# Optimization experiments

Measured on AMD Instinct MI355X. Metric: run time of the kernel, lower is better.

The kernel has to match this reference:

```python
import jax, jax.numpy as jnp
import numpy as np


def _prelu(x, alpha):
    # PReLU with alpha shared over H,W (per-channel alpha, shape (C,))
    return jnp.where(x >= 0, x, alpha * x)


def _maxpool_2x2_s1_same(x):
    # TF MaxPooling2D(pool_size=2, strides=1, padding='same'): pad bottom/right
    return jax.lax.reduce_window(
        x, -jnp.inf, jax.lax.max,
        window_dimensions=(1, 2, 2, 1), window_strides=(1, 1, 1, 1),
        padding=[(0, 0), (0, 1), (0, 1), (0, 0)])


def _down_sample(x, W, b, alpha):
    # 1x1 Conv2D stride 2 'same' == subsample then channel matmul
    y = jnp.einsum('bhwc,cd->bhwd', x[:, ::2, ::2, :], W) + b
    y = _prelu(y, alpha)
    return _maxpool_2x2_s1_same(y)


def _up_sample(x, W, b, alpha):
    # 1x1 Conv2DTranspose stride 2 'same': even positions get conv output, rest only bias
    B, H, Wd, C = x.shape
    y = jnp.einsum('bhwc,cd->bhwd', x, W)
    z = jnp.zeros((B, 2 * H, 2 * Wd, C), dtype=x.dtype).at[:, ::2, ::2, :].set(y) + b
    z = _prelu(z, alpha)
    return _maxpool_2x2_s1_same(z)


def setup_inputs() -> dict:
    key = jax.random.key(0)
    ks = jax.random.split(key, 12)
    B, H, C = 8, 512, 3
    return {
        'input1': jax.random.normal(ks[0], (B, 2 * H, 2 * H, C), jnp.float32),
        'input2': jax.random.normal(ks[1], (B, H, H, C), jnp.float32),
        'input3': jax.random.normal(ks[2], (B, H // 2, H // 2, C), jnp.float32),
        'W_down': jax.random.normal(ks[3], (C, C), jnp.float32) * 0.5,
        'b_down': jax.random.normal(ks[4], (C,), jnp.float32) * 0.1,
        'alpha_down': jax.random.uniform(ks[5], (C,), jnp.float32) * 0.25,
        'W_up': jax.random.normal(ks[6], (C, C), jnp.float32) * 0.5,
        'b_up': jax.random.normal(ks[7], (C,), jnp.float32) * 0.1,
        'alpha_up': jax.random.uniform(ks[8], (C,), jnp.float32) * 0.25,
        'W_c': jax.random.normal(ks[9], (C, C), jnp.float32) * 0.5,
        'b_c': jax.random.normal(ks[10], (C,), jnp.float32) * 0.1,
        'alpha_g': jax.random.uniform(ks[11], (C,), jnp.float32) * 0.25,
        'scale': 2,
    }


def reference(input1, input2, input3, W_down, b_down, alpha_down,
              W_up, b_up, alpha_up, W_c, b_c, alpha_g, scale):
    assert scale == 2, 'only scale=2 path is well-defined in the source'
    i1 = _down_sample(input1, W_down, b_down, alpha_down)  # (B,H,W,C)
    i2 = input2
    i3 = _up_sample(input3, W_up, b_up, alpha_up)          # (B,H,W,C)

    s = i1 + i2 + i3
    g = jnp.mean(s, axis=(1, 2), keepdims=True)            # GlobalAvgPool, (B,1,1,C)

    conv1x1 = lambda t: jnp.einsum('bhwc,cd->bhwd', t, W_c) + b_c
    x = _prelu(conv1x1(g), alpha_g)
    # self.conv2d is the SAME layer applied three times -> c1 == c2 == c3,
    # hence y1 == y2 == y3; compute once (identical math).
    y = jax.nn.softmax(conv1x1(x), axis=-1)                # (B,1,1,C)
    return y * i1 + y * i2 + y * i3
```

## Files before the change

kernel.cpp:

```cpp
#include <hip/hip_runtime.h>

#define HW 512
#define PITCH 200

__device__ __forceinline__ float prelu(float x, float a) { return x >= 0.f ? x : a * x; }

template<int MODE>
__global__ __launch_bounds__(256, 4) void pass_kernel(
    const float* __restrict__ in1, const float* __restrict__ in2, const float* __restrict__ in3,
    const float* __restrict__ Wd, const float* __restrict__ bd, const float* __restrict__ ad,
    const float* __restrict__ Wu, const float* __restrict__ bu, const float* __restrict__ au,
    float* __restrict__ partials,
    const float* __restrict__ Wc, const float* __restrict__ bc, const float* __restrict__ ag,
    float* __restrict__ out)
{
    __shared__ float d1[17 * PITCH];
    __shared__ float red[4][3];
    __shared__ float ybuf[3];

    const int tid   = threadIdx.x;
    const int bx    = blockIdx.x;
    const int by    = blockIdx.y;
    const int batch = blockIdx.z;
    const int h0    = by * 16;
    const int w0b   = bx * 64;

    if (MODE == 1 && tid < 64) {
        const float* pw = partials + batch * 256 * 3;
        float g0 = 0.f, g1 = 0.f, g2 = 0.f;
        #pragma unroll
        for (int k = 0; k < 4; ++k) {
            const float* p = pw + (tid + 64 * k) * 3;
            g0 += p[0]; g1 += p[1]; g2 += p[2];
        }
        #pragma unroll
        for (int off = 32; off > 0; off >>= 1) {
            g0 += __shfl_down(g0, off);
            g1 += __shfl_down(g1, off);
            g2 += __shfl_down(g2, off);
        }
        if (tid == 0) {
            const float inv_n = 1.f / (float)(HW * HW);
            g0 *= inv_n; g1 *= inv_n; g2 *= inv_n;
            const float x0 = prelu(g0 * Wc[0] + g1 * Wc[3] + g2 * Wc[6] + bc[0], ag[0]);
            const float x1 = prelu(g0 * Wc[1] + g1 * Wc[4] + g2 * Wc[7] + bc[1], ag[1]);
            const float x2 = prelu(g0 * Wc[2] + g1 * Wc[5] + g2 * Wc[8] + bc[2], ag[2]);
            const float q0 = x0 * Wc[0] + x1 * Wc[3] + x2 * Wc[6] + bc[0];
            const float q1 = x0 * Wc[1] + x1 * Wc[4] + x2 * Wc[7] + bc[1];
            const float q2 = x0 * Wc[2] + x1 * Wc[5] + x2 * Wc[8] + bc[2];
            const float m  = fmaxf(q0, fmaxf(q1, q2));
            const float e0 = expf(q0 - m), e1 = expf(q1 - m), e2 = expf(q2 - m);
            const float inv = 1.f / (e0 + e1 + e2);
            ybuf[0] = e0 * inv; ybuf[1] = e1 * inv; ybuf[2] = e2 * inv;
        }
    }

    float wd[9], wu[9];
    #pragma unroll
    for (int k = 0; k < 9; k++) { wd[k] = Wd[k]; wu[k] = Wu[k]; }
    const float bd0 = bd[0], bd1 = bd[1], bd2 = bd[2];
    const float ad0 = ad[0], ad1 = ad[1], ad2 = ad[2];
    const float bu0 = bu[0], bu1 = bu[1], bu2 = bu[2];
    const float au0 = au[0], au1 = au[1], au2 = au[2];
    const float cu0 = prelu(bu0, au0), cu1 = prelu(bu1, au1), cu2 = prelu(bu2, au2);

    #pragma unroll
    for (int step = 0; step < 2; ++step) {
        const int r = step ? 16 : (tid >> 4);
        const int g = step ? tid : (tid & 15);
        if (step == 0 || tid < 16) {
            const int gh  = h0 + r;
            const int ghc = gh < HW ? gh : (HW - 1);
            const float* rb = in1 + ((size_t)(batch * 1024 + 2 * ghc)) * 3072;
            const int px0 = 2 * w0b + 8 * g;
            const float4* lp = reinterpret_cast<const float4*>(rb + (size_t)px0 * 3);
            float arr[28];
            #pragma unroll
            for (int k = 0; k < 7; ++k)
                *reinterpret_cast<float4*>(&arr[4 * k]) = lp[k];

            const bool rowOOR = (gh >= HW);
            float* q = d1 + r * PITCH + 12 * g;
            #pragma unroll
            for (int j = 0; j < 4; ++j) {
                const float x0 = arr[6 * j], x1 = arr[6 * j + 1], x2 = arr[6 * j + 2];
                float v0 = prelu(x0 * wd[0] + x1 * wd[3] + x2 * wd[6] + bd0, ad0);
                float v1 = prelu(x0 * wd[1] + x1 * wd[4] + x2 * wd[7] + bd1, ad1);
                float v2 = prelu(x0 * wd[2] + x1 * wd[5] + x2 * wd[8] + bd2, ad2);
                q[3 * j + 0] = rowOOR ? -INFINITY : v0;
                q[3 * j + 1] = rowOOR ? -INFINITY : v1;
                q[3 * j + 2] = rowOOR ? -INFINITY : v2;
            }
            if (g == 15) {
                const float x0 = arr[24], x1 = arr[25], x2 = arr[26];
                float v0 = prelu(x0 * wd[0] + x1 * wd[3] + x2 * wd[6] + bd0, ad0);
                float v1 = prelu(x0 * wd[1] + x1 * wd[4] + x2 * wd[7] + bd1, ad1);
                float v2 = prelu(x0 * wd[2] + x1 * wd[5] + x2 * wd[8] + bd2, ad2);
                const bool oor = rowOOR || (w0b + 64 >= HW);
                q[12] = oor ? -INFINITY : v0;
                q[13] = oor ? -INFINITY : v1;
                q[14] = oor ? -INFINITY : v2;
            }
        }
    }
    __syncthreads();

    const int r  = tid >> 4;
    const int cg = tid & 15;
    const int h  = h0 + r;
    const int w0 = w0b + cg * 4;

    const float* in2p = in2 + ((size_t)((batch * HW + h) * HW + w0)) * 3;
    float i2v[12];
    #pragma unroll
    for (int k = 0; k < 3; ++k)
        *reinterpret_cast<float4*>(&i2v[4 * k]) = reinterpret_cast<const float4*>(in2p)[k];

    const int he  = h + (h & 1);
    const bool rOK = he < HW;
    const int hr3 = rOK ? (he >> 1) : 255;
    const int w3  = w0 >> 1;
    float ur[9];
    #pragma unroll
    for (int k = 0; k < 3; ++k) {
        const int wc = (w3 + k < 256) ? (w3 + k) : 255;
        const float* p = in3 + ((size_t)(batch * 256 + hr3) * 256 + wc) * 3;
        ur[3 * k + 0] = p[0]; ur[3 * k + 1] = p[1]; ur[3 * k + 2] = p[2];
    }
    float ud[3][3];
    #pragma unroll
    for (int k = 0; k < 3; ++k) {
        const bool ok = rOK && (w3 + k < 256);
        const float x0 = ur[3 * k], x1 = ur[3 * k + 1], x2 = ur[3 * k + 2];
        const float u0 = prelu(x0 * wu[0] + x1 * wu[3] + x2 * wu[6] + bu0, au0);
        const float u1 = prelu(x0 * wu[1] + x1 * wu[4] + x2 * wu[7] + bu1, au1);
        const float u2 = prelu(x0 * wu[2] + x1 * wu[5] + x2 * wu[8] + bu2, au2);
        ud[k][0] = ok ? fmaxf(cu0, u0) : cu0;
        ud[k][1] = ok ? fmaxf(cu1, u1) : cu1;
        ud[k][2] = ok ? fmaxf(cu2, u2) : cu2;
    }

    const int baseA = r * PITCH + cg * 12;
    const int baseB = baseA + PITCH;
    float pA0 = d1[baseA + 0], pA1 = d1[baseA + 1], pA2 = d1[baseA + 2];
    float pB0 = d1[baseB + 0], pB1 = d1[baseB + 1], pB2 = d1[baseB + 2];

    float s[4][3];
    #pragma unroll
    for (int j = 0; j < 4; ++j) {
        const int o = 3 * (j + 1);
        const float cA0 = d1[baseA + o], cA1 = d1[baseA + o + 1], cA2 = d1[baseA + o + 2];
        const float cB0 = d1[baseB + o], cB1 = d1[baseB + o + 1], cB2 = d1[baseB + o + 2];
        const int uk = (j + 1) >> 1;
        s[j][0] = fmaxf(fmaxf(pA0, cA0), fmaxf(pB0, cB0)) + i2v[3 * j + 0] + ud[uk][0];
        s[j][1] = fmaxf(fmaxf(pA1, cA1), fmaxf(pB1, cB1)) + i2v[3 * j + 1] + ud[uk][1];
        s[j][2] = fmaxf(fmaxf(pA2, cA2), fmaxf(pB2, cB2)) + i2v[3 * j + 2] + ud[uk][2];
        pA0 = cA0; pA1 = cA1; pA2 = cA2;
        pB0 = cB0; pB1 = cB1; pB2 = cB2;
    }

    if (MODE == 0) {
        float sum0 = s[0][0] + s[1][0] + s[2][0] + s[3][0];
        float sum1 = s[0][1] + s[1][1] + s[2][1] + s[3][1];
        float sum2 = s[0][2] + s[1][2] + s[2][2] + s[3][2];
        #pragma unroll
        for (int off = 32; off > 0; off >>= 1) {
            sum0 += __shfl_down(sum0, off);
            sum1 += __shfl_down(sum1, off);
            sum2 += __shfl_down(sum2, off);
        }
        if ((tid & 63) == 0) { red[tid >> 6][0] = sum0; red[tid >> 6][1] = sum1; red[tid >> 6][2] = sum2; }
        __syncthreads();
        if (tid == 0) {
            const int pid = (batch * 32 + by) * 8 + bx;
            partials[pid * 3 + 0] = red[0][0] + red[1][0] + red[2][0] + red[3][0];
            partials[pid * 3 + 1] = red[0][1] + red[1][1] + red[2][1] + red[3][1];
            partials[pid * 3 + 2] = red[0][2] + red[1][2] + red[2][2] + red[3][2];
        }
    } else {
        const float ym[3] = { ybuf[0], ybuf[1], ybuf[2] };
        float* outp = out + ((size_t)((batch * HW + h) * HW + w0)) * 3;
        #pragma unroll
        for (int k = 0; k < 3; ++k) {
            float4 v;
            v.x = s[(4 * k + 0) / 3][(4 * k + 0) % 3] * ym[(4 * k + 0) % 3];
            v.y = s[(4 * k + 1) / 3][(4 * k + 1) % 3] * ym[(4 * k + 1) % 3];
            v.z = s[(4 * k + 2) / 3][(4 * k + 2) % 3] * ym[(4 * k + 2) % 3];
            v.w = s[(4 * k + 3) / 3][(4 * k + 3) % 3] * ym[(4 * k + 3) % 3];
            reinterpret_cast<float4*>(outp)[k] = v;
        }
    }
}

extern "C" void kernel_launch(void* const* d_in, const int* in_sizes, int n_in,
                              void* d_out, int out_size, void* d_ws, size_t ws_size,
                              hipStream_t stream)
{
    const float* in1 = (const float*)d_in[0];
    const float* in2 = (const float*)d_in[1];
    const float* in3 = (const float*)d_in[2];
    const float* Wd  = (const float*)d_in[3];
    const float* bd  = (const float*)d_in[4];
    const float* ad  = (const float*)d_in[5];
    const float* Wu  = (const float*)d_in[6];
    const float* bu  = (const float*)d_in[7];
    const float* au  = (const float*)d_in[8];
    const float* Wc  = (const float*)d_in[9];
    const float* bc  = (const float*)d_in[10];
    const float* ag  = (const float*)d_in[11];
    float* out = (float*)d_out;
    float* partials = (float*)d_ws;

    pass_kernel<0><<<dim3(8, 32, 8), 256, 0, stream>>>(in1, in2, in3, Wd, bd, ad, Wu, bu, au,
                                                       partials, Wc, bc, ag, out);
    pass_kernel<1><<<dim3(8, 32, 8), 256, 0, stream>>>(in1, in2, in3, Wd, bd, ad, Wu, bu, au,
                                                       partials, Wc, bc, ag, out);
}
```

Before: 38.96 us.

## Materialize s once and apply gate in a separate elementwise scaling kernel

Instead of recomputing the downsample, upsample and sum from all three inputs in a second pass, the first kernel now writes the summed tensor s to the output buffer while also producing per-block partial sums. A second lightweight kernel reduces the partials, computes the softmax gate per batch, and rescales the stored s in place. This replaces a second full read of the large inputs with a read-modify-write of the output-sized buffer. The cost is an extra output write and read, which could partly hit in the last-level cache.

```diff
diff --git a/kernel.cpp b/kernel.cpp
--- a/kernel.cpp
+++ b/kernel.cpp
@@ -5,18 +5,14 @@
 
 __device__ __forceinline__ float prelu(float x, float a) { return x >= 0.f ? x : a * x; }
 
-template<int MODE>
-__global__ __launch_bounds__(256, 4) void pass_kernel(
+__global__ __launch_bounds__(256) void k1_compute_s(
     const float* __restrict__ in1, const float* __restrict__ in2, const float* __restrict__ in3,
     const float* __restrict__ Wd, const float* __restrict__ bd, const float* __restrict__ ad,
     const float* __restrict__ Wu, const float* __restrict__ bu, const float* __restrict__ au,
-    float* __restrict__ partials,
-    const float* __restrict__ Wc, const float* __restrict__ bc, const float* __restrict__ ag,
-    float* __restrict__ out)
+    float* __restrict__ s_out, float* __restrict__ partials)
 {
     __shared__ float d1[17 * PITCH];
     __shared__ float red[4][3];
-    __shared__ float ybuf[3];
 
     const int tid   = threadIdx.x;
     const int bx    = blockIdx.x;
@@ -24,36 +20,6 @@
     const int batch = blockIdx.z;
     const int h0    = by * 16;
     const int w0b   = bx * 64;
-
-    if (MODE == 1 && tid < 64) {
-        const float* pw = partials + batch * 256 * 3;
-        float g0 = 0.f, g1 = 0.f, g2 = 0.f;
-        #pragma unroll
-        for (int k = 0; k < 4; ++k) {
-            const float* p = pw + (tid + 64 * k) * 3;
-            g0 += p[0]; g1 += p[1]; g2 += p[2];
-        }
-        #pragma unroll
-        for (int off = 32; off > 0; off >>= 1) {
-            g0 += __shfl_down(g0, off);
-            g1 += __shfl_down(g1, off);
-            g2 += __shfl_down(g2, off);
-        }
-        if (tid == 0) {
-            const float inv_n = 1.f / (float)(HW * HW);
-            g0 *= inv_n; g1 *= inv_n; g2 *= inv_n;
-            const float x0 = prelu(g0 * Wc[0] + g1 * Wc[3] + g2 * Wc[6] + bc[0], ag[0]);
-            const float x1 = prelu(g0 * Wc[1] + g1 * Wc[4] + g2 * Wc[7] + bc[1], ag[1]);
-            const float x2 = prelu(g0 * Wc[2] + g1 * Wc[5] + g2 * Wc[8] + bc[2], ag[2]);
-            const float q0 = x0 * Wc[0] + x1 * Wc[3] + x2 * Wc[6] + bc[0];
-            const float q1 = x0 * Wc[1] + x1 * Wc[4] + x2 * Wc[7] + bc[1];
-            const float q2 = x0 * Wc[2] + x1 * Wc[5] + x2 * Wc[8] + bc[2];
-            const float m  = fmaxf(q0, fmaxf(q1, q2));
-            const float e0 = expf(q0 - m), e1 = expf(q1 - m), e2 = expf(q2 - m);
-            const float inv = 1.f / (e0 + e1 + e2);
-            ybuf[0] = e0 * inv; ybuf[1] = e1 * inv; ybuf[2] = e2 * inv;
-        }
-    }
 
     float wd[9], wu[9];
     #pragma unroll
@@ -159,36 +125,91 @@
         pB0 = cB0; pB1 = cB1; pB2 = cB2;
     }
 
-    if (MODE == 0) {
-        float sum0 = s[0][0] + s[1][0] + s[2][0] + s[3][0];
-        float sum1 = s[0][1] + s[1][1] + s[2][1] + s[3][1];
-        float sum2 = s[0][2] + s[1][2] + s[2][2] + s[3][2];
+    float* outp = s_out + ((size_t)((batch * HW + h) * HW + w0)) * 3;
+    #pragma unroll
+    for (int k = 0; k < 3; ++k) {
+        float4 v;
+        v.x = s[(4 * k + 0) / 3][(4 * k + 0) % 3];
+        v.y = s[(4 * k + 1) / 3][(4 * k + 1) % 3];
+        v.z = s[(4 * k + 2) / 3][(4 * k + 2) % 3];
+        v.w = s[(4 * k + 3) / 3][(4 * k + 3) % 3];
+        reinterpret_cast<float4*>(outp)[k] = v;
+    }
+
+    float sum0 = s[0][0] + s[1][0] + s[2][0] + s[3][0];
+    float sum1 = s[0][1] + s[1][1] + s[2][1] + s[3][1];
+    float sum2 = s[0][2] + s[1][2] + s[2][2] + s[3][2];
+    #pragma unroll
+    for (int off = 32; off > 0; off >>= 1) {
+        sum0 += __shfl_down(sum0, off);
+        sum1 += __shfl_down(sum1, off);
+        sum2 += __shfl_down(sum2, off);
+    }
+    if ((tid & 63) == 0) { red[tid >> 6][0] = sum0; red[tid >> 6][1] = sum1; red[tid >> 6][2] = sum2; }
+    __syncthreads();
+    if (tid == 0) {
+        const int pid = (batch * 32 + by) * 8 + bx;
+        partials[pid * 3 + 0] = red[0][0] + red[1][0] + red[2][0] + red[3][0];
+        partials[pid * 3 + 1] = red[0][1] + red[1][1] + red[2][1] + red[3][1];
+        partials[pid * 3 + 2] = red[0][2] + red[1][2] + red[2][2] + red[3][2];
+    }
+}
+
+__global__ __launch_bounds__(256) void k2_gate_scale(
+    const float* __restrict__ partials,
+    const float* __restrict__ Wc, const float* __restrict__ bc, const float* __restrict__ ag,
+    float* __restrict__ out)
+{
+    __shared__ float ybuf[3];
+    const int bid   = blockIdx.x;
+    const int batch = bid >> 7;
+    const int chunk = bid & 127;
+    const int tid   = threadIdx.x;
+
+    float* p = out + ((size_t)batch * 262144 + chunk * 2048 + tid * 8) * 3;
+    float4 v[6];
+    #pragma unroll
+    for (int k = 0; k < 6; ++k) v[k] = reinterpret_cast<float4*>(p)[k];
+
+    if (tid < 64) {
+        const float* pw = partials + batch * 256 * 3;
+        float g0 = 0.f, g1 = 0.f, g2 = 0.f;
+        #pragma unroll
+        for (int k = 0; k < 4; ++k) {
+            const float* q = pw + (tid + 64 * k) * 3;
+            g0 += q[0]; g1 += q[1]; g2 += q[2];
+        }
         #pragma unroll
         for (int off = 32; off > 0; off >>= 1) {
-            sum0 += __shfl_down(sum0, off);
-            sum1 += __shfl_down(sum1, off);
-            sum2 += __shfl_down(sum2, off);
-        }
-        if ((tid & 63) == 0) { red[tid >> 6][0] = sum0; red[tid >> 6][1] = sum1; red[tid >> 6][2] = sum2; }
-        __syncthreads();
+            g0 += __shfl_down(g0, off);
+            g1 += __shfl_down(g1, off);
+            g2 += __shfl_down(g2, off);
+        }
         if (tid == 0) {
-            const int pid = (batch * 32 + by) * 8 + bx;
-            partials[pid * 3 + 0] = red[0][0] + red[1][0] + red[2][0] + red[3][0];
-            partials[pid * 3 + 1] = red[0][1] + red[1][1] + red[2][1] + red[3][1];
-            partials[pid * 3 + 2] = red[0][2] + red[1][2] + red[2][2] + red[3][2];
-        }
-    } else {
-        const float ym[3] = { ybuf[0], ybuf[1], ybuf[2] };
-        float* outp = out + ((size_t)((batch * HW + h) * HW + w0)) * 3;
-        #pragma unroll
-        for (int k = 0; k < 3; ++k) {
-            float4 v;
-            v.x = s[(4 * k + 0) / 3][(4 * k + 0) % 3] * ym[(4 * k + 0) % 3];
-            v.y = s[(4 * k + 1) / 3][(4 * k + 1) % 3] * ym[(4 * k + 1) % 3];
-            v.z = s[(4 * k + 2) / 3][(4 * k + 2) % 3] * ym[(4 * k + 2) % 3];
-            v.w = s[(4 * k + 3) / 3][(4 * k + 3) % 3] * ym[(4 * k + 3) % 3];
-            reinterpret_cast<float4*>(outp)[k] = v;
-        }
+            const float inv_n = 1.f / (float)(HW * HW);
+            g0 *= inv_n; g1 *= inv_n; g2 *= inv_n;
+            const float x0 = prelu(g0 * Wc[0] + g1 * Wc[3] + g2 * Wc[6] + bc[0], ag[0]);
+            const float x1 = prelu(g0 * Wc[1] + g1 * Wc[4] + g2 * Wc[7] + bc[1], ag[1]);
+            const float x2 = prelu(g0 * Wc[2] + g1 * Wc[5] + g2 * Wc[8] + bc[2], ag[2]);
+            const float q0 = x0 * Wc[0] + x1 * Wc[3] + x2 * Wc[6] + bc[0];
+            const float q1 = x0 * Wc[1] + x1 * Wc[4] + x2 * Wc[7] + bc[1];
+            const float q2 = x0 * Wc[2] + x1 * Wc[5] + x2 * Wc[8] + bc[2];
+            const float m  = fmaxf(q0, fmaxf(q1, q2));
+            const float e0 = expf(q0 - m), e1 = expf(q1 - m), e2 = expf(q2 - m);
+            const float inv = 1.f / (e0 + e1 + e2);
+            ybuf[0] = e0 * inv; ybuf[1] = e1 * inv; ybuf[2] = e2 * inv;
+        }
+    }
+    __syncthreads();
+    const float ym[3] = { ybuf[0], ybuf[1], ybuf[2] };
+
+    #pragma unroll
+    for (int k = 0; k < 6; ++k) {
+        v[k].x *= ym[(4 * k + 0) % 3];
+        v[k].y *= ym[(4 * k + 1) % 3];
+        v[k].z *= ym[(4 * k + 2) % 3];
+        v[k].w *= ym[(4 * k + 3) % 3];
+        reinterpret_cast<float4*>(p)[k] = v[k];
     }
 }
 
@@ -211,8 +232,6 @@
     float* out = (float*)d_out;
     float* partials = (float*)d_ws;
 
-    pass_kernel<0><<<dim3(8, 32, 8), 256, 0, stream>>>(in1, in2, in3, Wd, bd, ad, Wu, bu, au,
-                                                       partials, Wc, bc, ag, out);
-    pass_kernel<1><<<dim3(8, 32, 8), 256, 0, stream>>>(in1, in2, in3, Wd, bd, ad, Wu, bu, au,
-                                                       partials, Wc, bc, ag, out);
+    k1_compute_s<<<dim3(8, 32, 8), 256, 0, stream>>>(in1, in2, in3, Wd, bd, ad, Wu, bu, au, out, partials);
+    k2_gate_scale<<<1024, 256, 0, stream>>>(partials, Wc, bc, ag, out);
 }
```

Measured after the change: 39.98 us. 1.03x slower.

## Fuse two passes into one kernel with per-batch spin-wait barrier

Applied to the files above, without the earlier changes.

Replaces the two-launch scheme, which recomputed the whole downsample/upsample sum in a second pass, with a single persistent-style kernel. Each block computes its tile once, publishes its partial sum, and spins on a per-batch atomic counter until all 128 blocks of that batch arrive, then scales its register-held values by the softmax weights and writes them out. Tiles are widened to 128 columns, which halves the block count to 1024. This removes the second read of all inputs, but it relies on every block of a batch being co-resident (1024 blocks of 256 threads) and adds a memset launch; otherwise it can deadlock.

```diff
diff --git a/kernel.cpp b/kernel.cpp
--- a/kernel.cpp
+++ b/kernel.cpp
@@ -1,18 +1,16 @@
 #include <hip/hip_runtime.h>
 
 #define HW 512
-#define PITCH 200
+#define PITCH 408
 
 __device__ __forceinline__ float prelu(float x, float a) { return x >= 0.f ? x : a * x; }
 
-template<int MODE>
-__global__ __launch_bounds__(256, 4) void pass_kernel(
+__global__ __launch_bounds__(256, 4) void fused_spin(
     const float* __restrict__ in1, const float* __restrict__ in2, const float* __restrict__ in3,
     const float* __restrict__ Wd, const float* __restrict__ bd, const float* __restrict__ ad,
     const float* __restrict__ Wu, const float* __restrict__ bu, const float* __restrict__ au,
-    float* __restrict__ partials,
     const float* __restrict__ Wc, const float* __restrict__ bc, const float* __restrict__ ag,
-    float* __restrict__ out)
+    int* __restrict__ cnt, float* __restrict__ partials, float* __restrict__ out)
 {
     __shared__ float d1[17 * PITCH];
     __shared__ float red[4][3];
@@ -23,15 +21,149 @@
     const int by    = blockIdx.y;
     const int batch = blockIdx.z;
     const int h0    = by * 16;
-    const int w0b   = bx * 64;
-
-    if (MODE == 1 && tid < 64) {
-        const float* pw = partials + batch * 256 * 3;
-        float g0 = 0.f, g1 = 0.f, g2 = 0.f;
-        #pragma unroll
-        for (int k = 0; k < 4; ++k) {
-            const float* p = pw + (tid + 64 * k) * 3;
-            g0 += p[0]; g1 += p[1]; g2 += p[2];
+    const int w0b   = bx * 128;
+
+    float wd[9], wu[9];
+    #pragma unroll
+    for (int k = 0; k < 9; k++) { wd[k] = Wd[k]; wu[k] = Wu[k]; }
+    const float bd0 = bd[0], bd1 = bd[1], bd2 = bd[2];
+    const float ad0 = ad[0], ad1 = ad[1], ad2 = ad[2];
+    const float bu0 = bu[0], bu1 = bu[1], bu2 = bu[2];
+    const float au0 = au[0], au1 = au[1], au2 = au[2];
+    const float cu0 = prelu(bu0, au0), cu1 = prelu(bu1, au1), cu2 = prelu(bu2, au2);
+
+    #pragma unroll
+    for (int step = 0; step < 2; ++step) {
+        const int r = step ? 16 : (tid >> 4);
+        const int g = step ? tid : (tid & 15);
+        if (step == 0 || tid < 16) {
+            const int gh  = h0 + r;
+            const int ghc = gh < HW ? gh : (HW - 1);
+            const float* rb = in1 + ((size_t)(batch * 1024 + 2 * ghc)) * 3072;
+            const int px0 = 2 * w0b + 16 * g;
+            const float4* lp = reinterpret_cast<const float4*>(rb + (size_t)px0 * 3);
+            float arr[52];
+            #pragma unroll
+            for (int k = 0; k < 13; ++k)
+                *reinterpret_cast<float4*>(&arr[4 * k]) = lp[k];
+
+            const bool rowOOR = (gh >= HW);
+            float* q = d1 + r * PITCH + 25 * g;
+            #pragma unroll
+            for (int j = 0; j < 8; ++j) {
+                const float x0 = arr[6 * j], x1 = arr[6 * j + 1], x2 = arr[6 * j + 2];
+                float v0 = prelu(x0 * wd[0] + x1 * wd[3] + x2 * wd[6] + bd0, ad0);
+                float v1 = prelu(x0 * wd[1] + x1 * wd[4] + x2 * wd[7] + bd1, ad1);
+                float v2 = prelu(x0 * wd[2] + x1 * wd[5] + x2 * wd[8] + bd2, ad2);
+                q[3 * j + 0] = rowOOR ? -INFINITY : v0;
+                q[3 * j + 1] = rowOOR ? -INFINITY : v1;
+                q[3 * j + 2] = rowOOR ? -INFINITY : v2;
+            }
+            if (g == 15) {
+                const float x0 = arr[48], x1 = arr[49], x2 = arr[50];
+                float v0 = prelu(x0 * wd[0] + x1 * wd[3] + x2 * wd[6] + bd0, ad0);
+                float v1 = prelu(x0 * wd[1] + x1 * wd[4] + x2 * wd[7] + bd1, ad1);
+                float v2 = prelu(x0 * wd[2] + x1 * wd[5] + x2 * wd[8] + bd2, ad2);
+                const bool oor = rowOOR || (w0b + 128 >= HW);
+                float* qh = d1 + r * PITCH + 400;
+                qh[0] = oor ? -INFINITY : v0;
+                qh[1] = oor ? -INFINITY : v1;
+                qh[2] = oor ? -INFINITY : v2;
+            }
+        }
+    }
+    __syncthreads();
+
+    const int r  = tid >> 4;
+    const int g  = tid & 15;
+    const int h  = h0 + r;
+    const int w0 = w0b + g * 8;
+
+    const float* in2p = in2 + ((size_t)((batch * HW + h) * HW + w0)) * 3;
+    float i2v[24];
+    #pragma unroll
+    for (int k = 0; k < 6; ++k)
+        *reinterpret_cast<float4*>(&i2v[4 * k]) = reinterpret_cast<const float4*>(in2p)[k];
+
+    const int he   = h + (h & 1);
+    const bool rOK = he < HW;
+    const int hr3  = rOK ? (he >> 1) : 255;
+    const int w3   = w0 >> 1;
+    float ur[15];
+    #pragma unroll
+    for (int k = 0; k < 5; ++k) {
+        const int wc = (w3 + k < 256) ? (w3 + k) : 255;
+        const float* p = in3 + ((size_t)(batch * 256 + hr3) * 256 + wc) * 3;
+        ur[3 * k + 0] = p[0]; ur[3 * k + 1] = p[1]; ur[3 * k + 2] = p[2];
+    }
+    float ud[5][3];
+    #pragma unroll
+    for (int k = 0; k < 5; ++k) {
+        const bool ok = rOK && (w3 + k < 256);
+        const float x0 = ur[3 * k], x1 = ur[3 * k + 1], x2 = ur[3 * k + 2];
+        const float u0 = prelu(x0 * wu[0] + x1 * wu[3] + x2 * wu[6] + bu0, au0);
+        const float u1 = prelu(x0 * wu[1] + x1 * wu[4] + x2 * wu[7] + bu1, au1);
+        const float u2 = prelu(x0 * wu[2] + x1 * wu[5] + x2 * wu[8] + bu2, au2);
+        ud[k][0] = ok ? fmaxf(cu0, u0) : cu0;
+        ud[k][1] = ok ? fmaxf(cu1, u1) : cu1;
+        ud[k][2] = ok ? fmaxf(cu2, u2) : cu2;
+    }
+
+    const int baseA = r * PITCH + 25 * g;
+    const int baseB = baseA + PITCH;
+    float pA0 = d1[baseA + 0], pA1 = d1[baseA + 1], pA2 = d1[baseA + 2];
+    float pB0 = d1[baseB + 0], pB1 = d1[baseB + 1], pB2 = d1[baseB + 2];
+
+    float s[8][3];
+    #pragma unroll
+    for (int j = 0; j < 8; ++j) {
+        const int o = 3 * (j + 1) + ((j + 1) >> 3);
+        const float cA0 = d1[baseA + o], cA1 = d1[baseA + o + 1], cA2 = d1[baseA + o + 2];
+        const float cB0 = d1[baseB + o], cB1 = d1[baseB + o + 1], cB2 = d1[baseB + o + 2];
+        const int uk = (j + 1) >> 1;
+        s[j][0] = fmaxf(fmaxf(pA0, cA0), fmaxf(pB0, cB0)) + i2v[3 * j + 0] + ud[uk][0];
+        s[j][1] = fmaxf(fmaxf(pA1, cA1), fmaxf(pB1, cB1)) + i2v[3 * j + 1] + ud[uk][1];
+        s[j][2] = fmaxf(fmaxf(pA2, cA2), fmaxf(pB2, cB2)) + i2v[3 * j + 2] + ud[uk][2];
+        pA0 = cA0; pA1 = cA1; pA2 = cA2;
+        pB0 = cB0; pB1 = cB1; pB2 = cB2;
+    }
+
+    float sum0 = 0.f, sum1 = 0.f, sum2 = 0.f;
+    #pragma unroll
+    for (int j = 0; j < 8; ++j) { sum0 += s[j][0]; sum1 += s[j][1]; sum2 += s[j][2]; }
+    #pragma unroll
+    for (int off = 32; off > 0; off >>= 1) {
+        sum0 += __shfl_down(sum0, off);
+        sum1 += __shfl_down(sum1, off);
+        sum2 += __shfl_down(sum2, off);
+    }
+    if ((tid & 63) == 0) { red[tid >> 6][0] = sum0; red[tid >> 6][1] = sum1; red[tid >> 6][2] = sum2; }
+    __syncthreads();
+    if (tid == 0) {
+        const int slot = batch * 128 + by * 4 + bx;
+        const float t0 = red[0][0] + red[1][0] + red[2][0] + red[3][0];
+        const float t1 = red[0][1] + red[1][1] + red[2][1] + red[3][1];
+        const float t2 = red[0][2] + red[1][2] + red[2][2] + red[3][2];
+        __hip_atomic_store(&partials[slot * 3 + 0], t0, __ATOMIC_RELAXED, __HIP_MEMORY_SCOPE_AGENT);
+        __hip_atomic_store(&partials[slot * 3 + 1], t1, __ATOMIC_RELAXED, __HIP_MEMORY_SCOPE_AGENT);
+        __hip_atomic_store(&partials[slot * 3 + 2], t2, __ATOMIC_RELAXED, __HIP_MEMORY_SCOPE_AGENT);
+        __hip_atomic_fetch_add(&cnt[batch], 1, __ATOMIC_RELEASE, __HIP_MEMORY_SCOPE_AGENT);
+        while (__hip_atomic_load(&cnt[batch], __ATOMIC_ACQUIRE, __HIP_MEMORY_SCOPE_AGENT) < 128)
+            __builtin_amdgcn_s_sleep(2);
+    }
+    __syncthreads();
+
+    if (tid < 64) {
+        const float* pw = partials + batch * 128 * 3;
+        float g0, g1, g2;
+        {
+            const int i0 = tid * 3, i1 = (tid + 64) * 3;
+            g0 = __hip_atomic_load(&pw[i0 + 0], __ATOMIC_RELAXED, __HIP_MEMORY_SCOPE_AGENT)
+               + __hip_atomic_load(&pw[i1 + 0], __ATOMIC_RELAXED, __HIP_MEMORY_SCOPE_AGENT);
+            g1 = __hip_atomic_load(&pw[i0 + 1], __ATOMIC_RELAXED, __HIP_MEMORY_SCOPE_AGENT)
+               + __hip_atomic_load(&pw[i1 + 1], __ATOMIC_RELAXED, __HIP_MEMORY_SCOPE_AGENT);
+            g2 = __hip_atomic_load(&pw[i0 + 2], __ATOMIC_RELAXED, __HIP_MEMORY_SCOPE_AGENT)
+               + __hip_atomic_load(&pw[i1 + 2], __ATOMIC_RELAXED, __HIP_MEMORY_SCOPE_AGENT);
         }
         #pragma unroll
         for (int off = 32; off > 0; off >>= 1) {
@@ -54,141 +186,18 @@
             ybuf[0] = e0 * inv; ybuf[1] = e1 * inv; ybuf[2] = e2 * inv;
         }
     }
-
-    float wd[9], wu[9];
-    #pragma unroll
-    for (int k = 0; k < 9; k++) { wd[k] = Wd[k]; wu[k] = Wu[k]; }
-    const float bd0 = bd[0], bd1 = bd[1], bd2 = bd[2];
-    const float ad0 = ad[0], ad1 = ad[1], ad2 = ad[2];
-    const float bu0 = bu[0], bu1 = bu[1], bu2 = bu[2];
-    const float au0 = au[0], au1 = au[1], au2 = au[2];
-    const float cu0 = prelu(bu0, au0), cu1 = prelu(bu1, au1), cu2 = prelu(bu2, au2);
-
-    #pragma unroll
-    for (int step = 0; step < 2; ++step) {
-        const int r = step ? 16 : (tid >> 4);
-        const int g = step ? tid : (tid & 15);
-        if (step == 0 || tid < 16) {
-            const int gh  = h0 + r;
-            const int ghc = gh < HW ? gh : (HW - 1);
-            const float* rb = in1 + ((size_t)(batch * 1024 + 2 * ghc)) * 3072;
-            const int px0 = 2 * w0b + 8 * g;
-            const float4* lp = reinterpret_cast<const float4*>(rb + (size_t)px0 * 3);
-            float arr[28];
-            #pragma unroll
-            for (int k = 0; k < 7; ++k)
-                *reinterpret_cast<float4*>(&arr[4 * k]) = lp[k];
-
-            const bool rowOOR = (gh >= HW);
-            float* q = d1 + r * PITCH + 12 * g;
-            #pragma unroll
-            for (int j = 0; j < 4; ++j) {
-                const float x0 = arr[6 * j], x1 = arr[6 * j + 1], x2 = arr[6 * j + 2];
-                float v0 = prelu(x0 * wd[0] + x1 * wd[3] + x2 * wd[6] + bd0, ad0);
-                float v1 = prelu(x0 * wd[1] + x1 * wd[4] + x2 * wd[7] + bd1, ad1);
-                float v2 = prelu(x0 * wd[2] + x1 * wd[5] + x2 * wd[8] + bd2, ad2);
-                q[3 * j + 0] = rowOOR ? -INFINITY : v0;
-                q[3 * j + 1] = rowOOR ? -INFINITY : v1;
-                q[3 * j + 2] = rowOOR ? -INFINITY : v2;
-            }
-            if (g == 15) {
-                const float x0 = arr[24], x1 = arr[25], x2 = arr[26];
-                float v0 = prelu(x0 * wd[0] + x1 * wd[3] + x2 * wd[6] + bd0, ad0);
-                float v1 = prelu(x0 * wd[1] + x1 * wd[4] + x2 * wd[7] + bd1, ad1);
-                float v2 = prelu(x0 * wd[2] + x1 * wd[5] + x2 * wd[8] + bd2, ad2);
-                const bool oor = rowOOR || (w0b + 64 >= HW);
-                q[12] = oor ? -INFINITY : v0;
-                q[13] = oor ? -INFINITY : v1;
-                q[14] = oor ? -INFINITY : v2;
-            }
-        }
-    }
-    __syncthreads();
-
-    const int r  = tid >> 4;
-    const int cg = tid & 15;
-    const int h  = h0 + r;
-    const int w0 = w0b + cg * 4;
-
-    const float* in2p = in2 + ((size_t)((batch * HW + h) * HW + w0)) * 3;
-    float i2v[12];
-    #pragma unroll
-    for (int k = 0; k < 3; ++k)
-        *reinterpret_cast<float4*>(&i2v[4 * k]) = reinterpret_cast<const float4*>(in2p)[k];
-
-    const int he  = h + (h & 1);
-    const bool rOK = he < HW;
-    const int hr3 = rOK ? (he >> 1) : 255;
-    const int w3  = w0 >> 1;
-    float ur[9];
-    #pragma unroll
-    for (int k = 0; k < 3; ++k) {
-        const int wc = (w3 + k < 256) ? (w3 + k) : 255;
-        const float* p = in3 + ((size_t)(batch * 256 + hr3) * 256 + wc) * 3;
-        ur[3 * k + 0] = p[0]; ur[3 * k + 1] = p[1]; ur[3 * k + 2] = p[2];
-    }
-    float ud[3][3];
-    #pragma unroll
-    for (int k = 0; k < 3; ++k) {
-        const bool ok = rOK && (w3 + k < 256);
-        const float x0 = ur[3 * k], x1 = ur[3 * k + 1], x2 = ur[3 * k + 2];
-        const float u0 = prelu(x0 * wu[0] + x1 * wu[3] + x2 * wu[6] + bu0, au0);
-        const float u1 = prelu(x0 * wu[1] + x1 * wu[4] + x2 * wu[7] + bu1, au1);
-        const float u2 = prelu(x0 * wu[2] + x1 * wu[5] + x2 * wu[8] + bu2, au2);
-        ud[k][0] = ok ? fmaxf(cu0, u0) : cu0;
-        ud[k][1] = ok ? fmaxf(cu1, u1) : cu1;
-        ud[k][2] = ok ? fmaxf(cu2, u2) : cu2;
-    }
-
-    const int baseA = r * PITCH + cg * 12;
-    const int baseB = baseA + PITCH;
-    float pA0 = d1[baseA + 0], pA1 = d1[baseA + 1], pA2 = d1[baseA + 2];
-    float pB0 = d1[baseB + 0], pB1 = d1[baseB + 1], pB2 = d1[baseB + 2];
-
-    float s[4][3];
-    #pragma unroll
-    for (int j = 0; j < 4; ++j) {
-        const int o = 3 * (j + 1);
-        const float cA0 = d1[baseA + o], cA1 = d1[baseA + o + 1], cA2 = d1[baseA + o + 2];
-        const float cB0 = d1[baseB + o], cB1 = d1[baseB + o + 1], cB2 = d1[baseB + o + 2];
-        const int uk = (j + 1) >> 1;
-        s[j][0] = fmaxf(fmaxf(pA0, cA0), fmaxf(pB0, cB0)) + i2v[3 * j + 0] + ud[uk][0];
-        s[j][1] = fmaxf(fmaxf(pA1, cA1), fmaxf(pB1, cB1)) + i2v[3 * j + 1] + ud[uk][1];
-        s[j][2] = fmaxf(fmaxf(pA2, cA2), fmaxf(pB2, cB2)) + i2v[3 * j + 2] + ud[uk][2];
-        pA0 = cA0; pA1 = cA1; pA2 = cA2;
-        pB0 = cB0; pB1 = cB1; pB2 = cB2;
-    }
-
-    if (MODE == 0) {
-        float sum0 = s[0][0] + s[1][0] + s[2][0] + s[3][0];
-        float sum1 = s[0][1] + s[1][1] + s[2][1] + s[3][1];
-        float sum2 = s[0][2] + s[1][2] + s[2][2] + s[3][2];
-        #pragma unroll
-        for (int off = 32; off > 0; off >>= 1) {
-            sum0 += __shfl_down(sum0, off);
-            sum1 += __shfl_down(sum1, off);
-            sum2 += __shfl_down(sum2, off);
-        }
-        if ((tid & 63) == 0) { red[tid >> 6][0] = sum0; red[tid >> 6][1] = sum1; red[tid >> 6][2] = sum2; }
-        __syncthreads();
-        if (tid == 0) {
-            const int pid = (batch * 32 + by) * 8 + bx;
-            partials[pid * 3 + 0] = red[0][0] + red[1][0] + red[2][0] + red[3][0];
-            partials[pid * 3 + 1] = red[0][1] + red[1][1] + red[2][1] + red[3][1];
-            partials[pid * 3 + 2] = red[0][2] + red[1][2] + red[2][2] + red[3][2];
-        }
-    } else {
-        const float ym[3] = { ybuf[0], ybuf[1], ybuf[2] };
-        float* outp = out + ((size_t)((batch * HW + h) * HW + w0)) * 3;
-        #pragma unroll
-        for (int k = 0; k < 3; ++k) {
-            float4 v;
-            v.x = s[(4 * k + 0) / 3][(4 * k + 0) % 3] * ym[(4 * k + 0) % 3];
-            v.y = s[(4 * k + 1) / 3][(4 * k + 1) % 3] * ym[(4 * k + 1) % 3];
-            v.z = s[(4 * k + 2) / 3][(4 * k + 2) % 3] * ym[(4 * k + 2) % 3];
-            v.w = s[(4 * k + 3) / 3][(4 * k + 3) % 3] * ym[(4 * k + 3) % 3];
-            reinterpret_cast<float4*>(outp)[k] = v;
-        }
+    __syncthreads();
+    const float ym[3] = { ybuf[0], ybuf[1], ybuf[2] };
+
+    float* outp = out + ((size_t)((batch * HW + h) * HW + w0)) * 3;
+    #pragma unroll
+    for (int k = 0; k < 6; ++k) {
+        float4 v;
+        v.x = s[(4 * k + 0) / 3][(4 * k + 0) % 3] * ym[(4 * k + 0) % 3];
+        v.y = s[(4 * k + 1) / 3][(4 * k + 1) % 3] * ym[(4 * k + 1) % 3];
+        v.z = s[(4 * k + 2) / 3][(4 * k + 2) % 3] * ym[(4 * k + 2) % 3];
+        v.w = s[(4 * k + 3) / 3][(4 * k + 3) % 3] * ym[(4 * k + 3) % 3];
+        reinterpret_cast<float4*>(outp)[k] = v;
     }
 }
 
@@ -209,10 +218,11 @@
     const float* bc  = (const float*)d_in[10];
     const float* ag  = (const float*)d_in[11];
     float* out = (float*)d_out;
-    float* partials = (float*)d_ws;
-
-    pass_kernel<0><<<dim3(8, 32, 8), 256, 0, stream>>>(in1, in2, in3, Wd, bd, ad, Wu, bu, au,
-                                                       partials, Wc, bc, ag, out);
-    pass_kernel<1><<<dim3(8, 32, 8), 256, 0, stream>>>(in1, in2, in3, Wd, bd, ad, Wu, bu, au,
-                                                       partials, Wc, bc, ag, out);
+
+    int*   cnt      = (int*)d_ws;
+    float* partials = (float*)((char*)d_ws + 64);
+
+    hipMemsetAsync(d_ws, 0, 64, stream);
+    fused_spin<<<dim3(4, 32, 8), 256, 0, stream>>>(in1, in2, in3, Wd, bd, ad, Wu, bu, au,
+                                                   Wc, bc, ag, cnt, partials, out);
 }
```

New measurement: 138.3 us. 3.55x slower.
